# Performance work log

Measured on AMD Instinct MI355X. Metric: run time of the kernel, lower is better.

The kernel has to match this reference:

```python
import jax, jax.numpy as jnp
import numpy as np

B, T, D = 32, 4096, 1024
LOG_T = False  # init_kwargs log_t


def setup_inputs() -> dict:
    key = jax.random.key(0)
    k1, k2 = jax.random.split(key)
    eh = jax.random.normal(k1, (B, T, D), dtype=jnp.float32)
    dhx = jax.random.normal(k2, (B, 1, D), dtype=jnp.float32)
    return {"eh": eh, "dhx": dhx}


def reference(eh, dhx):
    # scores: elementwise mult + reduce over feature dim -> [B, T]
    pax = jnp.sum(eh * dhx, axis=2)
    if LOG_T:
        pax = jnp.log(jnp.float32(pax.shape[1])) * pax
    ax = jax.nn.softmax(pax, axis=1)          # [B, T]
    # context: weighted sum over time -> [B, 1, D]
    sx = jnp.sum(eh * ax[:, :, None], axis=1, keepdims=True)
    return (sx, ax)
```

## Files before the change

kernel.cpp:

```cpp
#include <hip/hip_runtime.h>
#include <math.h>

#define NB 32
#define NT 4096
#define ND 1024
#define SPANS 4

typedef float f32x4 __attribute__((ext_vector_type(4)));


#define LOAD2(P, S_) do {                                                     \
    const f32x4* er0_ = ehb + (size_t)(row0 + 2*(S_)) * (ND/4);               \
    const f32x4* er1_ = er0_ + (ND/4);                                        \
    P##_e0 = er0_[0*64+lane]; P##_e1 = er0_[1*64+lane];                       \
    P##_e2 = er0_[2*64+lane]; P##_e3 = er0_[3*64+lane];                       \
    P##_f0 = er1_[0*64+lane]; P##_f1 = er1_[1*64+lane];                       \
    P##_f2 = er1_[2*64+lane]; P##_f3 = er1_[3*64+lane];                       \
} while (0)

#define COMPUTE2(P, S_) do {                                                  \
    f32x4 p0_ = P##_e0*dv0 + P##_e1*dv1 + P##_e2*dv2 + P##_e3*dv3;            \
    f32x4 p1_ = P##_f0*dv0 + P##_f1*dv1 + P##_f2*dv2 + P##_f3*dv3;            \
    float s0_ = p0_.x + p0_.y + p0_.z + p0_.w;                                \
    float s1_ = p1_.x + p1_.y + p1_.z + p1_.w;                                \
    _Pragma("unroll")                                                         \
    for (int off_ = 32; off_ > 0; off_ >>= 1) {                               \
        s0_ += __shfl_xor(s0_, off_, 64);                                     \
        s1_ += __shfl_xor(s1_, off_, 64);                                     \
    }                                                                         \
    if (lane == 0) {                                                          \
        s_pax[wave * rows_per_wave + 2*(S_)]     = s0_;                       \
        s_pax[wave * rows_per_wave + 2*(S_) + 1] = s1_;                       \
    }                                                                         \
    const float mn_ = fmaxf(m, fmaxf(s0_, s1_));                              \
    const float sc_ = __expf(m  - mn_);                                       \
    const float w0_ = __expf(s0_ - mn_);                                      \
    const float w1_ = __expf(s1_ - mn_);                                      \
    m = mn_;                                                                  \
    l = l*sc_ + w0_ + w1_;                                                    \
    a0 = a0*sc_ + w0_*P##_e0 + w1_*P##_f0;                                    \
    a1 = a1*sc_ + w0_*P##_e1 + w1_*P##_f1;                                    \
    a2 = a2*sc_ + w0_*P##_e2 + w1_*P##_f2;                                    \
    a3 = a3*sc_ + w0_*P##_e3 + w1_*P##_f3;                                    \
} while (0)

__global__ __launch_bounds__(256) void prodattn_pass1(
    const float* __restrict__ eh,
    const float* __restrict__ dhx,
    float* __restrict__ pax_out,
    float* __restrict__ ctx_out,
    float* __restrict__ m_out,
    float* __restrict__ l_out,
    int chunks, int rows_per_wave)
{
    const int chunk = blockIdx.x;
    const int b     = blockIdx.y;
    const int tid   = threadIdx.x;
    const int wave  = tid >> 6;
    const int lane  = tid & 63;

    __shared__ float s_pax[512];

    const f32x4* dhx4 = reinterpret_cast<const f32x4*>(dhx + (size_t)b * ND);
    const f32x4 dv0 = dhx4[0*64 + lane];
    const f32x4 dv1 = dhx4[1*64 + lane];
    const f32x4 dv2 = dhx4[2*64 + lane];
    const f32x4 dv3 = dhx4[3*64 + lane];

    f32x4 a0 = (f32x4)(0.f), a1 = (f32x4)(0.f), a2 = (f32x4)(0.f), a3 = (f32x4)(0.f);
    float m = -INFINITY, l = 0.f;

    const int row0 = chunk * (rows_per_wave * 4) + wave * rows_per_wave;
    const f32x4* ehb = reinterpret_cast<const f32x4*>(eh + (size_t)b * NT * ND);

    f32x4 A_e0, A_e1, A_e2, A_e3, A_f0, A_f1, A_f2, A_f3;
    f32x4 B_e0, B_e1, B_e2, B_e3, B_f0, B_f1, B_f2, B_f3;

    const int S = rows_per_wave >> 1;

    LOAD2(A, 0);
    int s = 0;
    for (; s + 2 < S; s += 2) {
        LOAD2(B, s + 1);
        COMPUTE2(A, s);
        LOAD2(A, s + 2);
        COMPUTE2(B, s + 1);
    }
    LOAD2(B, S - 1);
    COMPUTE2(A, S - 2);
    COMPUTE2(B, S - 1);

    __shared__ float  s_m[4];
    __shared__ float  s_l[4];
    __shared__ f32x4 s_acc[4][ND / 4];

    if (lane == 0) s_m[wave] = m;
    __syncthreads();

    {
        const int row_base = chunk * (rows_per_wave * 4);
        float* paxb = pax_out + (size_t)b * NT + row_base;
        const int n = rows_per_wave * 4;
        for (int j = tid; j < n; j += 256) paxb[j] = s_pax[j];
    }

    const float M = fmaxf(fmaxf(s_m[0], s_m[1]), fmaxf(s_m[2], s_m[3]));
    const float f = __expf(m - M);
    if (lane == 0) s_l[wave] = l * f;

    a0 *= f; a1 *= f; a2 *= f; a3 *= f;
    s_acc[wave][0*64 + lane] = a0;
    s_acc[wave][1*64 + lane] = a1;
    s_acc[wave][2*64 + lane] = a2;
    s_acc[wave][3*64 + lane] = a3;
    __syncthreads();

    f32x4 r = s_acc[0][tid] + s_acc[1][tid] + s_acc[2][tid] + s_acc[3][tid];

    reinterpret_cast<f32x4*>(ctx_out + ((size_t)b * chunks + chunk) * ND)[tid] = r;
    if (tid == 0) {
        m_out[b * chunks + chunk] = M;
        l_out[b * chunks + chunk] = s_l[0] + s_l[1] + s_l[2] + s_l[3];
    }
}

__global__ __launch_bounds__(256) void prodattn_pass2(
    float* __restrict__ sx_out,
    float* __restrict__ ax_inout,
    const float* __restrict__ ctx,
    const float* __restrict__ m_arr,
    const float* __restrict__ l_arr,
    int chunks)
{
    const int b    = blockIdx.x;
    const int role = blockIdx.y;
    const int tid  = threadIdx.x;
    const int wave = tid >> 6;
    const int lane = tid & 63;

    __shared__ float sM, sInv;
    if (wave == 0) {
        float mv = (lane < chunks) ? m_arr[b * chunks + lane] : -INFINITY;
        float lv = (lane < chunks) ? l_arr[b * chunks + lane] : 0.f;
        float M = mv;
        #pragma unroll
        for (int off = 32; off > 0; off >>= 1)
            M = fmaxf(M, __shfl_xor(M, off, 64));
        float c = lv * __expf(mv - M);
        #pragma unroll
        for (int off = 32; off > 0; off >>= 1)
            c += __shfl_xor(c, off, 64);
        if (lane == 0) { sM = M; sInv = 1.0f / c; }
    }
    __syncthreads();
    const float M   = sM;
    const float inv = sInv;

    if (role < SPANS) {
        f32x4* ax4 = reinterpret_cast<f32x4*>(ax_inout + (size_t)b * NT)
                     + role * (NT / 4 / SPANS);
        f32x4 v = ax4[tid];
        v.x = __expf(v.x - M) * inv;
        v.y = __expf(v.y - M) * inv;
        v.z = __expf(v.z - M) * inv;
        v.w = __expf(v.w - M) * inv;
        ax4[tid] = v;
    } else {
        const f32x4* cb = reinterpret_cast<const f32x4*>(ctx + (size_t)b * chunks * ND);
        const float* mb = m_arr + b * chunks;
        f32x4 acc0 = (f32x4)(0.f), acc1 = (f32x4)(0.f), acc2 = (f32x4)(0.f), acc3 = (f32x4)(0.f);
        int c = 0;
        for (; c + 3 < chunks; c += 4) {
            const float w0 = __expf(mb[c+0] - M);
            const float w1 = __expf(mb[c+1] - M);
            const float w2 = __expf(mb[c+2] - M);
            const float w3 = __expf(mb[c+3] - M);
            acc0 += w0 * cb[(size_t)(c+0)*(ND/4) + tid];
            acc1 += w1 * cb[(size_t)(c+1)*(ND/4) + tid];
            acc2 += w2 * cb[(size_t)(c+2)*(ND/4) + tid];
            acc3 += w3 * cb[(size_t)(c+3)*(ND/4) + tid];
        }
        for (; c < chunks; ++c) {
            const float w = __expf(mb[c] - M);
            acc0 += w * cb[(size_t)c*(ND/4) + tid];
        }
        f32x4 r = (acc0 + acc1 + acc2 + acc3) * inv;
        reinterpret_cast<f32x4*>(sx_out + (size_t)b * ND)[tid] = r;
    }
}

extern "C" void kernel_launch(void* const* d_in, const int* in_sizes, int n_in,
                              void* d_out, int out_size, void* d_ws, size_t ws_size,
                              hipStream_t stream) {
    const float* eh  = (const float*)d_in[0];
    const float* dhx = (const float*)d_in[1];

    float* out = (float*)d_out;
    float* sx  = out;
    float* ax  = out + NB * ND;

    int chunks = 16;
    while (chunks > 1 &&
           (size_t)NB * chunks * (ND + 2) * sizeof(float) > ws_size)
        chunks >>= 1;

    float* ctx   = (float*)d_ws;
    float* m_arr = ctx + (size_t)NB * chunks * ND;
    float* l_arr = m_arr + (size_t)NB * chunks;

    const int rows_per_wave = NT / (chunks * 4);

    dim3 grid1(chunks, NB);
    prodattn_pass1<<<grid1, 256, 0, stream>>>(eh, dhx, ax, ctx, m_arr, l_arr,
                                              chunks, rows_per_wave);
    dim3 grid2(NB, SPANS + 1);
    prodattn_pass2<<<grid2, 256, 0, stream>>>(sx, ax, ctx, m_arr, l_arr, chunks);
}
```

Measured before the change: 105.5 us.

## Fuse softmax finalize into pass1 via last-block atomic counter

Merges the two kernels into one: each chunk block bumps a per-batch atomic counter after a threadfence, and the last block for each batch normalizes the scores and combines the partial contexts. This removes the second kernel launch and its dependency gap. In exchange it adds a memset launch to reset the counters, and the tail work now runs serially in one block per batch instead of being spread across several blocks.

```diff
diff --git a/kernel.cpp b/kernel.cpp
--- a/kernel.cpp
+++ b/kernel.cpp
@@ -4,7 +4,6 @@
 #define NB 32
 #define NT 4096
 #define ND 1024
-#define SPANS 4
 
 typedef float f32x4 __attribute__((ext_vector_type(4)));
 
@@ -44,13 +43,15 @@
     a3 = a3*sc_ + w0_*P##_e3 + w1_*P##_f3;                                    \
 } while (0)
 
-__global__ __launch_bounds__(256) void prodattn_pass1(
+__global__ __launch_bounds__(256) void prodattn_fused(
     const float* __restrict__ eh,
     const float* __restrict__ dhx,
-    float* __restrict__ pax_out,
+    float* __restrict__ sx_out,
+    float* __restrict__ ax_out,
     float* __restrict__ ctx_out,
     float* __restrict__ m_out,
     float* __restrict__ l_out,
+    unsigned int* __restrict__ count,
     int chunks, int rows_per_wave)
 {
     const int chunk = blockIdx.x;
@@ -99,7 +100,7 @@
 
     {
         const int row_base = chunk * (rows_per_wave * 4);
-        float* paxb = pax_out + (size_t)b * NT + row_base;
+        float* paxb = ax_out + (size_t)b * NT + row_base;
         const int n = rows_per_wave * 4;
         for (int j = tid; j < n; j += 256) paxb[j] = s_pax[j];
     }
@@ -122,70 +123,71 @@
         m_out[b * chunks + chunk] = M;
         l_out[b * chunks + chunk] = s_l[0] + s_l[1] + s_l[2] + s_l[3];
     }
-}
-
-__global__ __launch_bounds__(256) void prodattn_pass2(
-    float* __restrict__ sx_out,
-    float* __restrict__ ax_inout,
-    const float* __restrict__ ctx,
-    const float* __restrict__ m_arr,
-    const float* __restrict__ l_arr,
-    int chunks)
-{
-    const int b    = blockIdx.x;
-    const int role = blockIdx.y;
-    const int tid  = threadIdx.x;
-    const int wave = tid >> 6;
-    const int lane = tid & 63;
+
+    __threadfence();
+    __syncthreads();
+    __shared__ int s_last;
+    if (tid == 0) {
+        const unsigned int old = atomicAdd(&count[b], 1u);
+        s_last = (old == (unsigned int)(chunks - 1)) ? 1 : 0;
+    }
+    __syncthreads();
+    if (!s_last) return;
+
+    __threadfence();
 
     __shared__ float sM, sInv;
     if (wave == 0) {
-        float mv = (lane < chunks) ? m_arr[b * chunks + lane] : -INFINITY;
-        float lv = (lane < chunks) ? l_arr[b * chunks + lane] : 0.f;
-        float M = mv;
+        float mv = (lane < chunks) ? m_out[b * chunks + lane] : -INFINITY;
+        float lv = (lane < chunks) ? l_out[b * chunks + lane] : 0.f;
+        float Mg = mv;
         #pragma unroll
         for (int off = 32; off > 0; off >>= 1)
-            M = fmaxf(M, __shfl_xor(M, off, 64));
-        float c = lv * __expf(mv - M);
+            Mg = fmaxf(Mg, __shfl_xor(Mg, off, 64));
+        float c = lv * __expf(mv - Mg);
         #pragma unroll
         for (int off = 32; off > 0; off >>= 1)
             c += __shfl_xor(c, off, 64);
-        if (lane == 0) { sM = M; sInv = 1.0f / c; }
-    }
-    __syncthreads();
-    const float M   = sM;
+        if (lane == 0) { sM = Mg; sInv = 1.0f / c; }
+    }
+    __syncthreads();
+    const float Mg  = sM;
     const float inv = sInv;
 
-    if (role < SPANS) {
-        f32x4* ax4 = reinterpret_cast<f32x4*>(ax_inout + (size_t)b * NT)
-                     + role * (NT / 4 / SPANS);
-        f32x4 v = ax4[tid];
-        v.x = __expf(v.x - M) * inv;
-        v.y = __expf(v.y - M) * inv;
-        v.z = __expf(v.z - M) * inv;
-        v.w = __expf(v.w - M) * inv;
-        ax4[tid] = v;
-    } else {
-        const f32x4* cb = reinterpret_cast<const f32x4*>(ctx + (size_t)b * chunks * ND);
-        const float* mb = m_arr + b * chunks;
+    {
+        f32x4* ax4 = reinterpret_cast<f32x4*>(ax_out + (size_t)b * NT);
+        #pragma unroll
+        for (int i = tid; i < NT / 4; i += 256) {
+            f32x4 v = ax4[i];
+            v.x = __expf(v.x - Mg) * inv;
+            v.y = __expf(v.y - Mg) * inv;
+            v.z = __expf(v.z - Mg) * inv;
+            v.w = __expf(v.w - Mg) * inv;
+            ax4[i] = v;
+        }
+    }
+
+    {
+        const f32x4* cb = reinterpret_cast<const f32x4*>(ctx_out + (size_t)b * chunks * ND);
+        const float* mb = m_out + b * chunks;
         f32x4 acc0 = (f32x4)(0.f), acc1 = (f32x4)(0.f), acc2 = (f32x4)(0.f), acc3 = (f32x4)(0.f);
         int c = 0;
         for (; c + 3 < chunks; c += 4) {
-            const float w0 = __expf(mb[c+0] - M);
-            const float w1 = __expf(mb[c+1] - M);
-            const float w2 = __expf(mb[c+2] - M);
-            const float w3 = __expf(mb[c+3] - M);
+            const float w0 = __expf(mb[c+0] - Mg);
+            const float w1 = __expf(mb[c+1] - Mg);
+            const float w2 = __expf(mb[c+2] - Mg);
+            const float w3 = __expf(mb[c+3] - Mg);
             acc0 += w0 * cb[(size_t)(c+0)*(ND/4) + tid];
             acc1 += w1 * cb[(size_t)(c+1)*(ND/4) + tid];
             acc2 += w2 * cb[(size_t)(c+2)*(ND/4) + tid];
             acc3 += w3 * cb[(size_t)(c+3)*(ND/4) + tid];
         }
         for (; c < chunks; ++c) {
-            const float w = __expf(mb[c] - M);
+            const float w = __expf(mb[c] - Mg);
             acc0 += w * cb[(size_t)c*(ND/4) + tid];
         }
-        f32x4 r = (acc0 + acc1 + acc2 + acc3) * inv;
-        reinterpret_cast<f32x4*>(sx_out + (size_t)b * ND)[tid] = r;
+        f32x4 r2 = (acc0 + acc1 + acc2 + acc3) * inv;
+        reinterpret_cast<f32x4*>(sx_out + (size_t)b * ND)[tid] = r2;
     }
 }
 
@@ -201,18 +203,19 @@
 
     int chunks = 16;
     while (chunks > 1 &&
-           (size_t)NB * chunks * (ND + 2) * sizeof(float) > ws_size)
+           (size_t)NB * (chunks * (ND + 2) + 1) * sizeof(float) > ws_size)
         chunks >>= 1;
 
     float* ctx   = (float*)d_ws;
     float* m_arr = ctx + (size_t)NB * chunks * ND;
     float* l_arr = m_arr + (size_t)NB * chunks;
+    unsigned int* count = (unsigned int*)(l_arr + (size_t)NB * chunks);
+
+    hipMemsetAsync(count, 0, NB * sizeof(unsigned int), stream);
 
     const int rows_per_wave = NT / (chunks * 4);
 
-    dim3 grid1(chunks, NB);
-    prodattn_pass1<<<grid1, 256, 0, stream>>>(eh, dhx, ax, ctx, m_arr, l_arr,
-                                              chunks, rows_per_wave);
-    dim3 grid2(NB, SPANS + 1);
-    prodattn_pass2<<<grid2, 256, 0, stream>>>(sx, ax, ctx, m_arr, l_arr, chunks);
+    dim3 grid(chunks, NB);
+    prodattn_fused<<<grid, 256, 0, stream>>>(eh, dhx, sx, ax, ctx, m_arr, l_arr,
+                                             count, chunks, rows_per_wave);
 }
```

Result: slower. 218.6 us (+107.2%).
